# Kernel optimization log

Measured on AMD Instinct MI355X. Metric: run time of the kernel, lower is better.

The kernel has to match this reference:

```python
import jax, jax.numpy as jnp
import numpy as np

D = 1024          # d_model
DQ = D // 4       # embedding dim (d_model//4)
DH = D // 2       # head hidden (d_model//2)
P = 6             # n_digit_positions = max_int_digits + n_decimal_digits
NOPS, NPT = 9, 10
B, T = 8, 2048


def _ln(x, g, b, eps=1e-5):
    m = jnp.mean(x, axis=-1, keepdims=True)
    v = jnp.mean(jnp.square(x - m), axis=-1, keepdims=True)
    return (x - m) * jax.lax.rsqrt(v + eps) * g + b


def _xavier(key, shape):
    fan_in, fan_out = shape[-2], shape[-1]
    lim = np.sqrt(6.0 / (fan_in + fan_out))
    return jax.random.uniform(key, shape, jnp.float32, -lim, lim)


def setup_inputs() -> dict:
    key = jax.random.key(0)
    ks = jax.random.split(key, 20)
    inp = {
        'hidden': jax.random.normal(ks[0], (B, T, D), jnp.float32),
        'operation_type': jax.random.randint(ks[1], (B,), 0, NOPS),
        'param_type': jax.random.randint(ks[2], (B, T), 0, NPT),
        # embeddings (std=0.02 like the torch init)
        'op_embed': 0.02 * jax.random.normal(ks[3], (NOPS, DQ), jnp.float32),
        'pt_embed': 0.02 * jax.random.normal(ks[4], (NPT, DQ), jnp.float32),
        'pos_embed': 0.02 * jax.random.normal(ks[5], (P, DQ), jnp.float32),
        # context_proj: Linear(D + D//2 -> D) + LayerNorm(D)
        'ctx_w': _xavier(ks[6], (D + D // 2, D)),
        'ctx_b': jnp.zeros((D,), jnp.float32),
        'ctx_g': jnp.ones((D,), jnp.float32),
        'ctx_beta': jnp.zeros((D,), jnp.float32),
        # sign_head: Linear(D->DH), LN(DH), Linear(DH->3)
        'sign_w1': _xavier(ks[7], (D, DH)),
        'sign_b1': jnp.zeros((DH,), jnp.float32),
        'sign_g': jnp.ones((DH,), jnp.float32),
        'sign_beta': jnp.zeros((DH,), jnp.float32),
        'sign_w2': _xavier(ks[8], (DH, 3)),
        'sign_b2': jnp.zeros((3,), jnp.float32),
        # digit heads stacked over positions: Linear(D+DQ->DH), LN(DH), Linear(DH->10)
        'dig_w1': _xavier(ks[9], (P, D + DQ, DH)),
        'dig_b1': jnp.zeros((P, DH), jnp.float32),
        'dig_g': jnp.ones((P, DH), jnp.float32),
        'dig_beta': jnp.zeros((P, DH), jnp.float32),
        'dig_w2': _xavier(ks[10], (P, DH, 10)),
        'dig_b2': jnp.zeros((P, 10), jnp.float32),
        'aux_w1': _xavier(ks[11], (D, DH)),
        'aux_b1': jnp.zeros((DH,), jnp.float32),
        'aux_w2': _xavier(ks[12], (DH, 1)),
        'aux_b2': jnp.zeros((1,), jnp.float32),
    }
    return inp


def reference(hidden, operation_type, param_type, op_embed, pt_embed, pos_embed,
              ctx_w, ctx_b, ctx_g, ctx_beta,
              sign_w1, sign_b1, sign_g, sign_beta, sign_w2, sign_b2,
              dig_w1, dig_b1, dig_g, dig_beta, dig_w2, dig_b2,
              aux_w1, aux_b1, aux_w2, aux_b2):
    b, t, d = hidden.shape
    gelu = lambda x: jax.nn.gelu(x, approximate=False)  # torch nn.GELU default

    op_emb = jnp.broadcast_to(op_embed[operation_type][:, None, :], (b, t, DQ))
    pm_emb = pt_embed[param_type]                       # [B,T,DQ]
    ctx_in = jnp.concatenate([hidden, op_emb, pm_emb], axis=-1)  # [B,T,1.5D]
    context = gelu(_ln(ctx_in @ ctx_w + ctx_b, ctx_g, ctx_beta))  # [B,T,D]

    sh = gelu(_ln(context @ sign_w1 + sign_b1, sign_g, sign_beta))
    sign_logits = sh @ sign_w2 + sign_b2                # [B,T,3]

    # digit heads, vectorized over position. concat(context, pos_emb[p]) @ W1
    # == context @ W1[:, :D] + pos_emb[p] @ W1[:, D:]
    h = (jnp.einsum('btd,pdh->btph', context, dig_w1[:, :D, :])
         + jnp.einsum('pq,pqh->ph', pos_embed, dig_w1[:, D:, :])
         + dig_b1)                                      # [B,T,P,DH]
    h = gelu(_ln(h, dig_g, dig_beta))
    digit_logits = jnp.einsum('btph,pho->btpo', h, dig_w2) + dig_b2  # [B,T,P,10]

    aux_value = gelu(context @ aux_w1 + aux_b1) @ aux_w2 + aux_b2    # [B,T,1]

    return sign_logits, digit_logits, aux_value
```

## Files before the change

kernel.cpp:

```cpp
#include <hip/hip_runtime.h>
#include <hip/hip_bf16.h>

typedef unsigned short u16;
typedef __attribute__((ext_vector_type(8))) __bf16 bf16x8;
typedef __attribute__((ext_vector_type(4))) float f32x4;

typedef __attribute__((address_space(1))) const void GVoid;
typedef __attribute__((address_space(3))) void LVoid;

__device__ __forceinline__ void async_load16(const u16* g, u16* l) {
    __builtin_amdgcn_global_load_lds((GVoid*)g, (LVoid*)l, 16, 0, 0);
}

__device__ __forceinline__ float bf2f(u16 u) {
    union { unsigned i; float f; } v; v.i = ((unsigned)u) << 16; return v.f;
}
__device__ __forceinline__ u16 f2bf(float f) {
    union { float f; unsigned i; } v; v.f = f;
    unsigned r = (v.i + 0x7FFFu + ((v.i >> 16) & 1u)) >> 16;
    return (u16)r;
}
__device__ __forceinline__ float gelu_f(float x) {
    float t = x * fmaf(0.0356774081f, x * x, 0.7978845608f);
    float e = __expf(2.0f * t);
    float r = 1.0f / (e + 1.0f);
    return x - x * r;
}

#define OP_E   0
#define PT_E   2304
#define POS_E  4864
#define CTX_B  6400
#define CTX_G  7424
#define CTX_BE 8448
#define S_B1   9472
#define S_G    9984
#define S_BE   10496
#define S_B2   11008
#define D_G    11012
#define D_BE   14084
#define D_B2   17156
#define A_B1   17216
#define A_B2   17728

struct SmallTab {
    const float* src[15];
    int off[15];
    int cnt[15];
};

__global__ __launch_bounds__(256) void convert_small(SmallTab tab, u16* __restrict__ dst)
{
    int idx = blockIdx.x * 256 + threadIdx.x;
#pragma unroll
    for (int e = 0; e < 15; ++e) {
        if (idx < tab.cnt[e]) {
            dst[tab.off[e] + idx] = f2bf(tab.src[e][idx]);
            return;
        }
        idx -= tab.cnt[e];
    }
}

__global__ __launch_bounds__(256) void convert_hidden(
    const float* __restrict__ src, u16* __restrict__ dst, int n8)
{
    int i = blockIdx.x * 256 + threadIdx.x;
    if (i >= n8) return;
    const float4* p = (const float4*)(src + (size_t)i * 8);
    float4 a = p[0], b = p[1];
    uint4 o;
    o.x = f2bf(a.x) | ((unsigned)f2bf(a.y) << 16);
    o.y = f2bf(a.z) | ((unsigned)f2bf(a.w) << 16);
    o.z = f2bf(b.x) | ((unsigned)f2bf(b.y) << 16);
    o.w = f2bf(b.z) | ((unsigned)f2bf(b.w) << 16);
    *(uint4*)(dst + (size_t)i * 8) = o;
}

__global__ __launch_bounds__(256) void transpose_all(
    const float* __restrict__ ctx_w, const float* __restrict__ sign_w1,
    const float* __restrict__ aux_w1, const float* __restrict__ dig_w1,
    u16* __restrict__ ctxWt, u16* __restrict__ BtAll)
{
    __shared__ u16 tl[32][33];
    int z = blockIdx.z;
    const float* src; u16* dst; size_t srcOff = 0; int srcLd, cols;
    if (z == 8) { src = ctx_w; dst = ctxWt; srcLd = 1024; cols = 1024; }
    else {
        srcLd = 512; cols = 512;
        if (z == 0) src = sign_w1;
        else if (z == 1) src = aux_w1;
        else { src = dig_w1; srcOff = (size_t)(z - 2) * 1280 * 512; }
        dst = BtAll + (size_t)z * 512 * 1024;
    }
    int n0 = blockIdx.x * 32;
    if (n0 >= cols) return;
    int k0 = blockIdx.y * 32;
    int t = threadIdx.x;
    int r = t >> 3;
    int c4 = (t & 7) * 4;
    float4 v = *(const float4*)&src[srcOff + (size_t)(k0 + r) * srcLd + n0 + c4];
    tl[r][c4 + 0] = f2bf(v.x); tl[r][c4 + 1] = f2bf(v.y);
    tl[r][c4 + 2] = f2bf(v.z); tl[r][c4 + 3] = f2bf(v.w);
    __syncthreads();
    ushort4 o;
    o.x = tl[c4 + 0][r]; o.y = tl[c4 + 1][r]; o.z = tl[c4 + 2][r]; o.w = tl[c4 + 3][r];
    *(ushort4*)&dst[(size_t)(n0 + r) * 1024 + k0 + c4] = o;
}

__global__ __launch_bounds__(256) void precompute_bias(
    const float* __restrict__ ctx_w, const float* __restrict__ dig_w1,
    const float* __restrict__ op_embed, const float* __restrict__ pt_embed,
    const float* __restrict__ pos_embed, const float* __restrict__ dig_b1,
    const int* __restrict__ op_type,
    float* __restrict__ E_op, float* __restrict__ P_pt, float* __restrict__ dbias)
{
    int idx = blockIdx.x * 256 + threadIdx.x;
    if (idx < 8192) {
        int b = idx >> 10, n = idx & 1023;
        const float* e = op_embed + op_type[b] * 256;
        float s = 0.f;
        for (int q = 0; q < 256; ++q)
            s += e[q] * ctx_w[(size_t)(1024 + q) * 1024 + n];
        E_op[idx] = s;
    } else if (idx < 18432) {
        int i = idx - 8192;
        int v = i >> 10, n = i & 1023;
        const float* e = pt_embed + v * 256;
        float s = 0.f;
        for (int q = 0; q < 256; ++q)
            s += e[q] * ctx_w[(size_t)(1280 + q) * 1024 + n];
        P_pt[i] = s;
    } else if (idx < 21504) {
        int i = idx - 18432;
        int p = i >> 9, h = i & 511;
        const float* e = pos_embed + p * 256;
        float s = dig_b1[p * 512 + h];
        for (int q = 0; q < 256; ++q)
            s += e[q] * dig_w1[(size_t)p * 1280 * 512 + (size_t)(1024 + q) * 512 + h];
        dbias[i] = s;
    }
}

__global__ __launch_bounds__(256) void build_vec(
    const u16* __restrict__ csm, const float* __restrict__ dbias,
    float* __restrict__ biasAll, float* __restrict__ gammaAll,
    float* __restrict__ betaAll)
{
    int n = blockIdx.x * 256 + threadIdx.x;
    float bi, g, be;
    if (n < 512) {
        bi = bf2f(csm[S_B1 + n]); g = bf2f(csm[S_G + n]); be = bf2f(csm[S_BE + n]);
    } else if (n < 1024) {
        bi = bf2f(csm[A_B1 + n - 512]); g = 1.f; be = 0.f;
    } else {
        int h = n - 1024;
        bi = dbias[h]; g = bf2f(csm[D_G + h]); be = bf2f(csm[D_BE + h]);
    }
    biasAll[n] = bi; gammaAll[n] = g; betaAll[n] = be;
}

__global__ __launch_bounds__(256) void build_w2pad(
    const float* __restrict__ sign_w2, const float* __restrict__ dig_w2,
    const float* __restrict__ aux_w2, u16* __restrict__ W2pad)
{
    int idx = blockIdx.x * 256 + threadIdx.x;
    int row = idx >> 12, k = idx & 4095;
    int r = row >> 4, o = row & 15;
    float v = 0.f;
    if (r == 0) {
        if (o < 3 && k < 512) v = sign_w2[k * 3 + o];
    } else if (r == 7) {
        if (o == 0 && k >= 512 && k < 1024) v = aux_w2[k - 512];
    } else {
        int p = r - 1, lo = 1024 + p * 512;
        if (o < 10 && k >= lo && k < lo + 512) v = dig_w2[(size_t)p * 5120 + (k - lo) * 10 + o];
    }
    W2pad[idx] = f2bf(v);
}

__global__ __launch_bounds__(256) void stats_fin(
    const float2* __restrict__ partials, float2* __restrict__ stats, int Rh)
{
    int i = blockIdx.x * 256 + threadIdx.x;
    if (i >= Rh * 8) return;
    int row = i >> 3, s = i & 7;
    float2 o;
    if (s == 1) {
        o = make_float2(0.f, 1.f);
    } else {
        float2 a = partials[(size_t)(2 * s) * Rh + row];
        float2 b = partials[(size_t)(2 * s + 1) * Rh + row];
        float sm = a.x + b.x, s2 = a.y + b.y;
        float mean = sm * (1.f / 512.f);
        float var = fmaxf(s2 * (1.f / 512.f) - mean * mean, 0.f);
        o = make_float2(mean, rsqrtf(var + 1e-5f));
    }
    stats[i] = o;
}

template<bool STATS>
__global__ __launch_bounds__(512) void gemm_8ph(
    const u16* __restrict__ A, const u16* __restrict__ Bt, u16* __restrict__ C,
    int M, int N, const float* __restrict__ biasAll, float2* __restrict__ partials)
{
    __shared__ u16 smem[65536];
    const int tid = threadIdx.x;
    const int wid = tid >> 6, lane = tid & 63;
    const int quad = lane >> 4, r16 = lane & 15;
    const int wm = wid >> 2, wn = wid & 3;

    const int Mtiles = M >> 8;
    int flat = blockIdx.x + blockIdx.y * gridDim.x;
    int cpx = (Mtiles * (N >> 8)) >> 3;
    int swz = (flat & 7) * cpx + (flat >> 3);
    int bm = swz % Mtiles, bn = swz / Mtiles;
    const int m0 = bm << 8, n0 = bn << 8;

    const int rb = tid >> 3;
    const int cx = ((tid & 7) ^ (rb & 7)) * 8;
    const u16* gA = A + (size_t)(m0 + rb) * 1024 + cx;
    const u16* gB = Bt + (size_t)(n0 + rb) * 1024 + cx;

#define STAGE(arr, h, tt) do { \
        u16* _d = smem + ((((tt) & 1) * 2 + (arr)) * 2 + (h)) * 8192 + wid * 512; \
        const u16* _s = ((arr) ? gB : gA) + (size_t)((h) * 128) * 1024 + (tt) * 64; \
        async_load16(_s, _d); \
        async_load16(_s + (size_t)64 * 1024, _d + 4096); \
    } while (0)

    STAGE(0, 0, 0); STAGE(0, 1, 0); STAGE(1, 0, 0); STAGE(1, 1, 0);
    STAGE(0, 0, 1); STAGE(0, 1, 1); STAGE(1, 0, 1);
    asm volatile("s_waitcnt vmcnt(6)" ::: "memory");
    asm volatile("s_barrier" ::: "memory");

    f32x4 acc[8][4] = {};
    const int kx0 = ((quad) ^ (r16 & 7)) * 8;
    const int kx1 = ((4 + quad) ^ (r16 & 7)) * 8;

#define QUAD(MF0, NF0) \
        _Pragma("unroll") \
        for (int ks = 0; ks < 2; ++ks) \
            _Pragma("unroll") \
            for (int mi = 0; mi < 4; ++mi) \
                _Pragma("unroll") \
                for (int nj = 0; nj < 2; ++nj) \
                    acc[(MF0) + mi][(NF0) + nj] = \
                        __builtin_amdgcn_mfma_f32_16x16x32_bf16( \
                            afr[(MF0) + mi][ks], bfr[(NF0) + nj][ks], \
                            acc[(MF0) + mi][(NF0) + nj], 0, 0, 0);

    for (int t = 0; t < 16; ++t) {
        const int cur = t & 1;
        const u16* sA = smem + cur * 32768 + wm * 8192 + r16 * 64;
        const u16* sB = smem + cur * 32768 + 16384 + (wn >> 1) * 8192
                        + ((wn & 1) * 64 + r16) * 64;

        if (t + 1 < 16) STAGE(1, 1, t + 1);
        bf16x8 afr[8][2], bfr[4][2];
#pragma unroll
        for (int mf = 0; mf < 8; ++mf) {
            afr[mf][0] = *(const bf16x8*)&sA[mf * 1024 + kx0];
            afr[mf][1] = *(const bf16x8*)&sA[mf * 1024 + kx1];
        }
#pragma unroll
        for (int nf = 0; nf < 4; ++nf) {
            bfr[nf][0] = *(const bf16x8*)&sB[nf * 1024 + kx0];
            bfr[nf][1] = *(const bf16x8*)&sB[nf * 1024 + kx1];
        }
        __builtin_amdgcn_s_setprio(1);
        QUAD(0, 0)
        __builtin_amdgcn_s_setprio(0);
        asm volatile("s_waitcnt lgkmcnt(0)" ::: "memory");
        __builtin_amdgcn_sched_barrier(0);
        asm volatile("s_barrier" ::: "memory");
        __builtin_amdgcn_sched_barrier(0);

        if (t + 2 < 16) STAGE(0, 0, t + 2);
        __builtin_amdgcn_sched_barrier(0);
        __builtin_amdgcn_s_setprio(1);
        QUAD(0, 2)
        __builtin_amdgcn_s_setprio(0);
        __builtin_amdgcn_sched_barrier(0);
        asm volatile("s_barrier" ::: "memory");
        __builtin_amdgcn_sched_barrier(0);

        if (t + 2 < 16) STAGE(0, 1, t + 2);
        __builtin_amdgcn_sched_barrier(0);
        __builtin_amdgcn_s_setprio(1);
        QUAD(4, 0)
        __builtin_amdgcn_s_setprio(0);
        __builtin_amdgcn_sched_barrier(0);
        asm volatile("s_barrier" ::: "memory");
        __builtin_amdgcn_sched_barrier(0);

        if (t + 2 < 16) STAGE(1, 0, t + 2);
        __builtin_amdgcn_sched_barrier(0);
        __builtin_amdgcn_s_setprio(1);
        QUAD(4, 2)
        __builtin_amdgcn_s_setprio(0);
        __builtin_amdgcn_sched_barrier(0);
        if (t < 14)       asm volatile("s_waitcnt vmcnt(6)" ::: "memory");
        else if (t == 14) asm volatile("s_waitcnt vmcnt(0)" ::: "memory");
        asm volatile("s_barrier" ::: "memory");
    }
#undef QUAD
#undef STAGE

    float bnf[4];
    float2* lds2 = (float2*)smem;
    int sstat = 0, prp = 0, parp = 0;
    if constexpr (STATS) {
#pragma unroll
        for (int nf = 0; nf < 4; ++nf)
            bnf[nf] = biasAll[n0 + wn * 64 + nf * 16 + r16];
        sstat = wn * 16 + r16; prp = sstat >> 1; parp = sstat & 1;
    }
#pragma unroll
    for (int mf = 0; mf < 8; ++mf) {
        u16 cvm[4][4];
#pragma unroll
        for (int nf = 0; nf < 4; ++nf)
#pragma unroll
            for (int r = 0; r < 4; ++r)
                cvm[nf][r] = f2bf(acc[mf][nf][r]);
        if constexpr (STATS) {
#pragma unroll
            for (int r = 0; r < 4; ++r) {
                float sv = 0.f, s2v = 0.f;
#pragma unroll
                for (int nf = 0; nf < 4; ++nf) {
                    float v = bf2f(cvm[nf][r]) + bnf[nf];
                    sv += v; s2v += v * v;
                }
                int lr = wm * 128 + mf * 16 + quad * 4 + r;
                int pp = ((prp + lr) & 31) * 2 + parp;
                lds2[lr * 64 + pp] = make_float2(sv, s2v);
            }
        }
#pragma unroll
        for (int nf = 0; nf < 4; ++nf) {
            size_t base = (size_t)(m0 + wm * 128 + mf * 16 + quad * 4) * N
                          + n0 + wn * 64 + nf * 16 + r16;
#pragma unroll
            for (int r = 0; r < 4; ++r)
                C[base + (size_t)r * N] = cvm[nf][r];
        }
    }
    if constexpr (STATS) {
        __syncthreads();
        int row = tid >> 1, half = tid & 1;
        float sv = 0.f, s2v = 0.f;
#pragma unroll
        for (int i = 0; i < 16; ++i) {
            int pp = ((half * 16 + i + row) & 31) * 2;
            f32x4 q = *(const f32x4*)&lds2[row * 64 + pp];
            sv += q[0] + q[2]; s2v += q[1] + q[3];
        }
        sv += __shfl_xor(sv, 1); s2v += __shfl_xor(s2v, 1);
        if (half == 0)
            partials[(size_t)bn * M + m0 + row] = make_float2(sv, s2v);
    }
}

__global__ __launch_bounds__(256) void ln_ctx_kernel(
    const u16* __restrict__ pre, const float* __restrict__ E_op,
    const float* __restrict__ P_pt, const int* __restrict__ ptype,
    const u16* __restrict__ csm, u16* __restrict__ ctx, int tokOff)
{
    __shared__ float red[8];
    int local = blockIdx.x;
    int token = tokOff + local;
    int b = token >> 11;
    int pt = ptype[token];
    int tid = threadIdx.x;
    int c = tid * 4;
    int wid = tid >> 6, lane = tid & 63;

    ushort4 xp = *(const ushort4*)&pre[(size_t)local * 1024 + c];
    float4 eo = *(const float4*)&E_op[b * 1024 + c];
    float4 pp = *(const float4*)&P_pt[pt * 1024 + c];
    ushort4 cb4 = *(const ushort4*)&csm[CTX_B + c];
    float x[4];
    x[0] = bf2f(xp.x) + eo.x + pp.x + bf2f(cb4.x);
    x[1] = bf2f(xp.y) + eo.y + pp.y + bf2f(cb4.y);
    x[2] = bf2f(xp.z) + eo.z + pp.z + bf2f(cb4.z);
    x[3] = bf2f(xp.w) + eo.w + pp.w + bf2f(cb4.w);

    float s = x[0] + x[1] + x[2] + x[3];
    float s2 = x[0]*x[0] + x[1]*x[1] + x[2]*x[2] + x[3]*x[3];
    for (int off = 32; off; off >>= 1) { s += __shfl_xor(s, off); s2 += __shfl_xor(s2, off); }
    if (lane == 0) { red[wid] = s; red[4 + wid] = s2; }
    __syncthreads();
    s  = red[0] + red[1] + red[2] + red[3];
    s2 = red[4] + red[5] + red[6] + red[7];
    float mean = s * (1.f / 1024.f);
    float var = fmaxf(s2 * (1.f / 1024.f) - mean * mean, 0.f);
    float rs = rsqrtf(var + 1e-5f);

    ushort4 g4 = *(const ushort4*)&csm[CTX_G + c];
    ushort4 b4 = *(const ushort4*)&csm[CTX_BE + c];
    ushort4 o;
    o.x = f2bf(gelu_f((x[0] - mean) * rs * bf2f(g4.x) + bf2f(b4.x)));
    o.y = f2bf(gelu_f((x[1] - mean) * rs * bf2f(g4.y) + bf2f(b4.y)));
    o.z = f2bf(gelu_f((x[2] - mean) * rs * bf2f(g4.z) + bf2f(b4.z)));
    o.w = f2bf(gelu_f((x[3] - mean) * rs * bf2f(g4.w) + bf2f(b4.w)));
    *(ushort4*)&ctx[(size_t)token * 1024 + c] = o;
}

__global__ __launch_bounds__(512) void gemm_final_fused(
    const u16* __restrict__ A, const u16* __restrict__ W2pad,
    const float* __restrict__ biasAll, const float* __restrict__ gammaAll,
    const float* __restrict__ betaAll, const float2* __restrict__ stats,
    const u16* __restrict__ csm, float* __restrict__ out, int tokOff)
{
    __shared__ u16 As[64 * 64];
    __shared__ u16 Bs[128 * 64];
    const int tid = threadIdx.x;
    const int wid = tid >> 6, lane = tid & 63;
    const int quad = lane >> 4, r16 = lane & 15;
    const int m0 = blockIdx.x * 64;

    const int r0 = tid >> 3;
    const int lg = tid & 7;
    const int c8 = lg * 8;
    const int pgA = ((lg ^ (r0 & 7)) * 8);
    const u16* arow = A + (size_t)(m0 + r0) * 4096;

    const int bcol = ((tid & 7) ^ (r0 & 7)) * 8;
    const u16* brow = W2pad + (size_t)r0 * 4096 + bcol;

    f32x4 acc[4] = {};

    uint4 xa = *(const uint4*)(arow + c8);

    for (int sl = 0; sl < 8; ++sl) {
        const float2 st = stats[(m0 + r0) * 8 + sl];
        for (int kb = 0; kb < 8; ++kb) {
            const int k0 = sl * 512 + kb * 64;
            async_load16(brow + k0, Bs + tid * 8);
            async_load16(brow + (size_t)64 * 4096 + k0, Bs + 4096 + tid * 8);
            uint4 xn = xa;
            if (k0 + 64 < 4096) xn = *(const uint4*)(arow + k0 + 64 + c8);
            const int kk = k0 + c8;
            float4 bi0 = *(const float4*)&biasAll[kk],  bi1 = *(const float4*)&biasAll[kk + 4];
            float4 g0  = *(const float4*)&gammaAll[kk], g1  = *(const float4*)&gammaAll[kk + 4];
            float4 be0 = *(const float4*)&betaAll[kk],  be1 = *(const float4*)&betaAll[kk + 4];
            float bb[8] = {bi0.x, bi0.y, bi0.z, bi0.w, bi1.x, bi1.y, bi1.z, bi1.w};
            float gg[8] = {g0.x, g0.y, g0.z, g0.w, g1.x, g1.y, g1.z, g1.w};
            float bt[8] = {be0.x, be0.y, be0.z, be0.w, be1.x, be1.y, be1.z, be1.w};
            u16 xr[8]; *(uint4*)&xr[0] = xa;
            u16 o[8];
#pragma unroll
            for (int j = 0; j < 8; ++j) {
                float v = (bf2f(xr[j]) + bb[j] - st.x) * st.y * gg[j] + bt[j];
                o[j] = f2bf(gelu_f(v));
            }
            *(uint4*)&As[r0 * 64 + pgA] = *(const uint4*)&o[0];
            __syncthreads();

            bf16x8 af[4][2], bw[2];
#pragma unroll
            for (int ks = 0; ks < 2; ++ks) {
                int pg = ((ks * 4 + quad) ^ (r16 & 7)) * 8;
#pragma unroll
                for (int i = 0; i < 4; ++i)
                    af[i][ks] = *(const bf16x8*)&As[(i * 16 + r16) * 64 + pg];
                bw[ks] = *(const bf16x8*)&Bs[(wid * 16 + r16) * 64 + pg];
            }
#pragma unroll
            for (int ks = 0; ks < 2; ++ks)
#pragma unroll
                for (int i = 0; i < 4; ++i)
                    acc[i] = __builtin_amdgcn_mfma_f32_16x16x32_bf16(
                        af[i][ks], bw[ks], acc[i], 0, 0, 0);
            __syncthreads();
            xa = xn;
        }
    }

    const int cg = wid, o = r16;
    int mode = -1; float obias = 0.f;
    if (cg == 0)      { if (o < 3)  { mode = 0; obias = bf2f(csm[S_B2 + o]); } }
    else if (cg == 7) { if (o == 0) { mode = 2; obias = bf2f(csm[A_B2]); } }
    else              { if (o < 10) { mode = 1; obias = bf2f(csm[D_B2 + (cg - 1) * 10 + o]); } }
    if (mode >= 0) {
#pragma unroll
        for (int i = 0; i < 4; ++i)
#pragma unroll
            for (int r = 0; r < 4; ++r) {
                int token = tokOff + m0 + i * 16 + quad * 4 + r;
                float v = acc[i][r] + obias;
                if (mode == 0)      out[(size_t)token * 3 + o] = v;
                else if (mode == 1) out[49152 + ((size_t)token * 6 + (cg - 1)) * 10 + o] = v;
                else                out[1032192 + (size_t)token] = v;
            }
    }
}

extern "C" void kernel_launch(void* const* d_in, const int* in_sizes, int n_in,
                              void* d_out, int out_size, void* d_ws, size_t ws_size,
                              hipStream_t stream) {
    const float* hidden    = (const float*)d_in[0];
    const int*   op_type   = (const int*)d_in[1];
    const int*   pt_type   = (const int*)d_in[2];
    const float* op_embed  = (const float*)d_in[3];
    const float* pt_embed  = (const float*)d_in[4];
    const float* pos_embed = (const float*)d_in[5];
    const float* ctx_w     = (const float*)d_in[6];
    const float* sign_w1   = (const float*)d_in[10];
    const float* sign_w2   = (const float*)d_in[14];
    const float* dig_w1    = (const float*)d_in[16];
    const float* dig_b1    = (const float*)d_in[17];
    const float* dig_w2    = (const float*)d_in[20];
    const float* aux_w1    = (const float*)d_in[22];
    const float* aux_w2    = (const float*)d_in[24];

    char* ws = (char*)d_ws;
    u16*    ctxWt    = (u16*)(ws + 0);
    u16*    BtAll    = (u16*)(ws + 2097152);
    float*  E_op     = (float*)(ws + 10485760);
    float*  P_pt     = (float*)(ws + 10518528);
    float*  dbias    = (float*)(ws + 10559488);
    u16*    csm      = (u16*)(ws + 10571776);
    float*  biasAll  = (float*)(ws + 10637312);
    float*  gammaAll = (float*)(ws + 10653696);
    float*  betaAll  = (float*)(ws + 10670080);
    float2* stats    = (float2*)(ws + 10686464);
    u16*    context  = (u16*)(ws + 11735040);
    u16*    scratch  = (u16*)(ws + 45289472);
    u16*    W2pad    = ctxWt;
    size_t S = (ws_size > 45289472) ? ws_size - 45289472 : 0;

    int Rc = 16384;
    while ((size_t)Rc * 2048 > S && Rc > 512) Rc >>= 1;
    int Rh = 16384;
    while ((size_t)Rh * 8320 > S && Rh > 256) Rh >>= 1;
    float2* partials = (float2*)((char*)scratch + (size_t)Rh * 8192);

    float* out = (float*)d_out;

    SmallTab tab;
    const float* srcs[15] = { op_embed, pt_embed, pos_embed,
                              (const float*)d_in[7], (const float*)d_in[8], (const float*)d_in[9],
                              (const float*)d_in[11], (const float*)d_in[12], (const float*)d_in[13],
                              (const float*)d_in[15],
                              (const float*)d_in[18], (const float*)d_in[19], (const float*)d_in[21],
                              (const float*)d_in[23], (const float*)d_in[25] };
    const int offs[15] = { OP_E, PT_E, POS_E, CTX_B, CTX_G, CTX_BE,
                           S_B1, S_G, S_BE, S_B2,
                           D_G, D_BE, D_B2, A_B1, A_B2 };
    const int cnts[15] = { 2304, 2560, 1536, 1024, 1024, 1024,
                           512, 512, 512, 3,
                           3072, 3072, 60, 512, 1 };
    for (int i = 0; i < 15; ++i) { tab.src[i] = srcs[i]; tab.off[i] = offs[i]; tab.cnt[i] = cnts[i]; }
    convert_small<<<70, 256, 0, stream>>>(tab, csm);

    transpose_all<<<dim3(32, 32, 9), 256, 0, stream>>>(
        ctx_w, sign_w1, aux_w1, dig_w1, ctxWt, BtAll);
    precompute_bias<<<84, 256, 0, stream>>>(
        ctx_w, dig_w1, op_embed, pt_embed, pos_embed, dig_b1, op_type,
        E_op, P_pt, dbias);
    build_vec<<<16, 256, 0, stream>>>(csm, dbias, biasAll, gammaAll, betaAll);

    u16* hbf16 = context;
    convert_hidden<<<8192, 256, 0, stream>>>(hidden, hbf16, 16384 * 1024 / 8);

    for (int t0 = 0; t0 < 16384; t0 += Rc) {
        gemm_8ph<false><<<dim3(Rc / 256, 4), 512, 0, stream>>>(
            hbf16 + (size_t)t0 * 1024, ctxWt, scratch, Rc, 1024, nullptr, nullptr);
        ln_ctx_kernel<<<Rc, 256, 0, stream>>>(
            scratch, E_op, P_pt, pt_type, csm, context, t0);
    }

    build_w2pad<<<2048, 256, 0, stream>>>(sign_w2, dig_w2, aux_w2, W2pad);

    for (int t0 = 0; t0 < 16384; t0 += Rh) {
        gemm_8ph<true><<<dim3(Rh / 256, 16), 512, 0, stream>>>(
            context + (size_t)t0 * 1024, BtAll, scratch, Rh, 4096,
            biasAll, partials);
        stats_fin<<<(Rh * 8 + 255) / 256, 256, 0, stream>>>(partials, stats, Rh);
        gemm_final_fused<<<Rh / 64, 512, 0, stream>>>(
            scratch, W2pad, biasAll, gammaAll, betaAll, stats, csm, out, t0);
    }
}
```

Before: 512.0 us.

## Use 2D XCD-aware tile partitioning and smaller blocks in final fused GEMM

The tile-to-block mapping in the main GEMM now splits the M×N tile grid into a PM×PN arrangement across the 8 XCD groups (flat&7), so each XCD works on a compact 2D region and reuses A and B tiles in its L2 better than the previous row-major chunking. The final fused GEMM shrinks from 64-row/512-thread blocks to 32-row/256-thread blocks with a 2×2 MFMA tile per wave, doubling the block count for better CU occupancy and balance. In exchange, each smaller block reloads the full W2pad tile per 32 rows, which doubles B traffic.

Measured after the change: 481.2 us. -6.0%, faster.

```diff
diff --git a/kernel.cpp b/kernel.cpp
--- a/kernel.cpp
+++ b/kernel.cpp
@@ -202,7 +202,8 @@
 template<bool STATS>
 __global__ __launch_bounds__(512) void gemm_8ph(
     const u16* __restrict__ A, const u16* __restrict__ Bt, u16* __restrict__ C,
-    int M, int N, const float* __restrict__ biasAll, float2* __restrict__ partials)
+    int M, int N, int PM, int PN,
+    const float* __restrict__ biasAll, float2* __restrict__ partials)
 {
     __shared__ u16 smem[65536];
     const int tid = threadIdx.x;
@@ -210,11 +211,13 @@
     const int quad = lane >> 4, r16 = lane & 15;
     const int wm = wid >> 2, wn = wid & 3;
 
-    const int Mtiles = M >> 8;
+    const int Mtiles = M >> 8, Ntiles = N >> 8;
     int flat = blockIdx.x + blockIdx.y * gridDim.x;
-    int cpx = (Mtiles * (N >> 8)) >> 3;
-    int swz = (flat & 7) * cpx + (flat >> 3);
-    int bm = swz % Mtiles, bn = swz / Mtiles;
+    int x = flat & 7, l = flat >> 3;
+    int Mloc = Mtiles / PM, Nloc = Ntiles / PN;
+    int xm = x / PN, xn = x - xm * PN;
+    int bm = xm * Mloc + l / Nloc;
+    int bn = xn * Nloc + l % Nloc;
     const int m0 = bm << 8, n0 = bn << 8;
 
     const int rb = tid >> 3;
@@ -408,18 +411,18 @@
     *(ushort4*)&ctx[(size_t)token * 1024 + c] = o;
 }
 
-__global__ __launch_bounds__(512) void gemm_final_fused(
+__global__ __launch_bounds__(256) void gemm_final_fused(
     const u16* __restrict__ A, const u16* __restrict__ W2pad,
     const float* __restrict__ biasAll, const float* __restrict__ gammaAll,
     const float* __restrict__ betaAll, const float2* __restrict__ stats,
     const u16* __restrict__ csm, float* __restrict__ out, int tokOff)
 {
-    __shared__ u16 As[64 * 64];
+    __shared__ u16 As[32 * 64];
     __shared__ u16 Bs[128 * 64];
     const int tid = threadIdx.x;
     const int wid = tid >> 6, lane = tid & 63;
     const int quad = lane >> 4, r16 = lane & 15;
-    const int m0 = blockIdx.x * 64;
+    const int m0 = blockIdx.x * 32;
 
     const int r0 = tid >> 3;
     const int lg = tid & 7;
@@ -430,7 +433,7 @@
     const int bcol = ((tid & 7) ^ (r0 & 7)) * 8;
     const u16* brow = W2pad + (size_t)r0 * 4096 + bcol;
 
-    f32x4 acc[4] = {};
+    f32x4 acc[2][2] = {};
 
     uint4 xa = *(const uint4*)(arow + c8);
 
@@ -438,8 +441,10 @@
         const float2 st = stats[(m0 + r0) * 8 + sl];
         for (int kb = 0; kb < 8; ++kb) {
             const int k0 = sl * 512 + kb * 64;
-            async_load16(brow + k0, Bs + tid * 8);
-            async_load16(brow + (size_t)64 * 4096 + k0, Bs + 4096 + tid * 8);
+#pragma unroll
+            for (int h = 0; h < 4; ++h)
+                async_load16(brow + (size_t)(h * 32) * 4096 + k0,
+                             Bs + h * 2048 + tid * 8);
             uint4 xn = xa;
             if (k0 + 64 < 4096) xn = *(const uint4*)(arow + k0 + 64 + c8);
             const int kk = k0 + c8;
@@ -459,42 +464,49 @@
             *(uint4*)&As[r0 * 64 + pgA] = *(const uint4*)&o[0];
             __syncthreads();
 
-            bf16x8 af[4][2], bw[2];
+            bf16x8 af[2][2], bw[2][2];
 #pragma unroll
             for (int ks = 0; ks < 2; ++ks) {
                 int pg = ((ks * 4 + quad) ^ (r16 & 7)) * 8;
 #pragma unroll
-                for (int i = 0; i < 4; ++i)
+                for (int i = 0; i < 2; ++i)
                     af[i][ks] = *(const bf16x8*)&As[(i * 16 + r16) * 64 + pg];
-                bw[ks] = *(const bf16x8*)&Bs[(wid * 16 + r16) * 64 + pg];
+#pragma unroll
+                for (int j = 0; j < 2; ++j)
+                    bw[j][ks] = *(const bf16x8*)&Bs[((wid * 2 + j) * 16 + r16) * 64 + pg];
             }
 #pragma unroll
             for (int ks = 0; ks < 2; ++ks)
 #pragma unroll
-                for (int i = 0; i < 4; ++i)
-                    acc[i] = __builtin_amdgcn_mfma_f32_16x16x32_bf16(
-                        af[i][ks], bw[ks], acc[i], 0, 0, 0);
+                for (int i = 0; i < 2; ++i)
+#pragma unroll
+                    for (int j = 0; j < 2; ++j)
+                        acc[i][j] = __builtin_amdgcn_mfma_f32_16x16x32_bf16(
+                            af[i][ks], bw[j][ks], acc[i][j], 0, 0, 0);
             __syncthreads();
             xa = xn;
         }
     }
 
-    const int cg = wid, o = r16;
-    int mode = -1; float obias = 0.f;
-    if (cg == 0)      { if (o < 3)  { mode = 0; obias = bf2f(csm[S_B2 + o]); } }
-    else if (cg == 7) { if (o == 0) { mode = 2; obias = bf2f(csm[A_B2]); } }
-    else              { if (o < 10) { mode = 1; obias = bf2f(csm[D_B2 + (cg - 1) * 10 + o]); } }
-    if (mode >= 0) {
-#pragma unroll
-        for (int i = 0; i < 4; ++i)
-#pragma unroll
-            for (int r = 0; r < 4; ++r) {
-                int token = tokOff + m0 + i * 16 + quad * 4 + r;
-                float v = acc[i][r] + obias;
-                if (mode == 0)      out[(size_t)token * 3 + o] = v;
-                else if (mode == 1) out[49152 + ((size_t)token * 6 + (cg - 1)) * 10 + o] = v;
-                else                out[1032192 + (size_t)token] = v;
-            }
+#pragma unroll
+    for (int j = 0; j < 2; ++j) {
+        const int cg = wid * 2 + j, o = r16;
+        int mode = -1; float obias = 0.f;
+        if (cg == 0)      { if (o < 3)  { mode = 0; obias = bf2f(csm[S_B2 + o]); } }
+        else if (cg == 7) { if (o == 0) { mode = 2; obias = bf2f(csm[A_B2]); } }
+        else              { if (o < 10) { mode = 1; obias = bf2f(csm[D_B2 + (cg - 1) * 10 + o]); } }
+        if (mode >= 0) {
+#pragma unroll
+            for (int i = 0; i < 2; ++i)
+#pragma unroll
+                for (int r = 0; r < 4; ++r) {
+                    int token = tokOff + m0 + i * 16 + quad * 4 + r;
+                    float v = acc[i][j][r] + obias;
+                    if (mode == 0)      out[(size_t)token * 3 + o] = v;
+                    else if (mode == 1) out[49152 + ((size_t)token * 6 + (cg - 1)) * 10 + o] = v;
+                    else                out[1032192 + (size_t)token] = v;
+                }
+        }
     }
 }
 
@@ -538,6 +550,11 @@
     while ((size_t)Rh * 8320 > S && Rh > 256) Rh >>= 1;
     float2* partials = (float2*)((char*)scratch + (size_t)Rh * 8192);
 
+    int PMh = 2, PNh = 4;
+    if (((Rh >> 8) & 1) != 0) { PMh = 1; PNh = 8; }
+    int PMc = 8, PNc = 1;
+    if (((Rc >> 8) % 8) != 0) { PMc = 2; PNc = 4; }
+
     float* out = (float*)d_out;
 
     SmallTab tab;
@@ -568,7 +585,8 @@
 
     for (int t0 = 0; t0 < 16384; t0 += Rc) {
         gemm_8ph<false><<<dim3(Rc / 256, 4), 512, 0, stream>>>(
-            hbf16 + (size_t)t0 * 1024, ctxWt, scratch, Rc, 1024, nullptr, nullptr);
+            hbf16 + (size_t)t0 * 1024, ctxWt, scratch, Rc, 1024, PMc, PNc,
+            nullptr, nullptr);
         ln_ctx_kernel<<<Rc, 256, 0, stream>>>(
             scratch, E_op, P_pt, pt_type, csm, context, t0);
     }
@@ -577,10 +595,10 @@
 
     for (int t0 = 0; t0 < 16384; t0 += Rh) {
         gemm_8ph<true><<<dim3(Rh / 256, 16), 512, 0, stream>>>(
-            context + (size_t)t0 * 1024, BtAll, scratch, Rh, 4096,
+            context + (size_t)t0 * 1024, BtAll, scratch, Rh, 4096, PMh, PNh,
             biasAll, partials);
         stats_fin<<<(Rh * 8 + 255) / 256, 256, 0, stream>>>(partials, stats, Rh);
-        gemm_final_fused<<<Rh / 64, 512, 0, stream>>>(
+        gemm_final_fused<<<Rh / 32, 256, 0, stream>>>(
             scratch, W2pad, biasAll, gammaAll, betaAll, stats, csm, out, t0);
     }
 }
```
